# Optimization experiments

Measured on AMD Instinct MI355X. Metric: run time of the kernel, lower is better.

Reference implementation:

```python
import jax, jax.numpy as jnp
import numpy as np

B, L = 16, 54            # dialogues, utterances per dialogue
NDIM = 512; H = 512; NS = 2
T = B * L                # 864 utterances
N = 3 * T                # 2592 nodes (l,a,v per utterance)
NE = B * (L + 3)         # 912 hyperedges (3 modality + L utterance per dialogue)
NNZ = 6 * T              # 5184 incidence entries
E = B * 3 * L * (L - 1)  # 137376 directed intra-modality edges
NUM_L = 3; NUM_K = 4
EPS = 1e-8


def _build_indices():
    rng = np.random.default_rng(0)
    spk = rng.integers(0, NS, size=(B, L))
    # qmask [L, B, NS] one-hot of speakers (matches torch argmax path)
    qmask = np.eye(NS, dtype=np.float32)[spk].transpose(1, 0, 2)
    ar = np.arange(L)
    i1, i2, ht = [], [], []
    for d in range(B):
        base = d * 3 * L
        nl = base + ar; na = nl + L; nv = nl + 2 * L
        # 3 modality hyperedges then L per-utterance (l,a,v) hyperedges
        i1 += [nl, na, nv, np.stack([nl, na, nv], 1).reshape(-1)]
        eb = d * (L + 3)
        i2 += [np.repeat(eb + np.arange(3), L), np.repeat(eb + 3 + ar, 3)]
        ht += [np.ones(L, np.int64), np.zeros(3, np.int64)]
    hyperedge_index = np.stack([np.concatenate(i1), np.concatenate(i2)]).astype(np.int64)
    hyperedge_type = np.concatenate(ht)
    # full permutation edges within each modality of each dialogue
    s0 = np.repeat(ar, L); d0 = np.tile(ar, L)
    m = s0 != d0; s0, d0 = s0[m], d0[m]
    src, dst, et = [], [], []
    for d in range(B):
        same = (spk[d][s0] == spk[d][d0]).astype(np.int64)
        for mm in range(3):
            off = d * 3 * L + mm * L
            src.append(s0 + off); dst.append(d0 + off); et.append(same)
    edge_index = np.stack([np.concatenate(src), np.concatenate(dst)]).astype(np.int64)
    edge_type = np.concatenate(et)
    return qmask, hyperedge_index, hyperedge_type, edge_index, edge_type


def setup_inputs() -> dict:
    key = jax.random.key(0)
    ks = jax.random.split(key, 16)
    qmask, hei, het, ei, et = _build_indices()
    n = lambda k, s: jax.random.normal(k, s, dtype=jnp.float32)
    inp = {
        'a': n(ks[0], (T, NDIM)), 'v': n(ks[1], (T, NDIM)), 'l': n(ks[2], (T, NDIM)),
        'qmask': jnp.asarray(qmask),
        'spk_emb': n(ks[3], (NS, NDIM)) * 0.05,
        'fc1_W': n(ks[4], (NDIM, H)) * 0.05, 'fc1_b': jnp.zeros((H,), jnp.float32),
        'he_weight': jnp.ones((NE,), jnp.float32),
        'ew_weight': jnp.ones((NNZ,), jnp.float32),
        'he_attr1': jax.random.uniform(ks[5], (H,), dtype=jnp.float32),
        'he_attr2': jax.random.uniform(ks[6], (H,), dtype=jnp.float32),
        'hc_W': n(ks[7], (NUM_L, H, H)) * 0.05, 'hc_b': jnp.zeros((NUM_L, H), jnp.float32),
        'm3_W0': n(ks[8], (NUM_K, H, H)) * 0.05,
        'm3_W1': n(ks[9], (NUM_K, H, H)) * 0.05,
        'm3_Wself': n(ks[10], (NUM_K, H, H)) * 0.05,
        'm3_b': jnp.zeros((NUM_K, H), jnp.float32),
        'hyperedge_index': jnp.asarray(hei), 'hyperedge_type': jnp.asarray(het),
        'edge_index': jnp.asarray(ei), 'edge_type': jnp.asarray(et),
    }
    return inp


def reference(a, v, l, qmask, spk_emb, fc1_W, fc1_b, he_weight, ew_weight,
              he_attr1, he_attr2, hc_W, hc_b, m3_W0, m3_W1, m3_Wself, m3_b,
              hyperedge_index, hyperedge_type, edge_index, edge_type):
    seg = jax.ops.segment_sum
    # speaker embedding added to text modality (equal dia_len -> simple transpose)
    qm = qmask.transpose(1, 0, 2).reshape(T, NS)
    l = l + spk_emb[jnp.argmax(qm, axis=-1)]
    # per-dialogue node order: [l_d ; a_d ; v_d]
    feats = jnp.concatenate([l.reshape(B, L, NDIM), a.reshape(B, L, NDIM),
                             v.reshape(B, L, NDIM)], axis=1).reshape(N, NDIM)
    x1 = feats @ fc1_W + fc1_b
    node_i, edge_i = hyperedge_index[0], hyperedge_index[1]
    tfl = hyperedge_type.astype(x1.dtype)[:, None]
    edge_attr = he_attr1[None, :] * tfl + he_attr2[None, :] * (1.0 - tfl)  # [NE,H]
    out = x1
    for ll in range(NUM_L):  # hypergraph conv: gather->edge agg->scatter->linear
        de = seg(ew_weight, edge_i, num_segments=NE)
        e = seg(ew_weight[:, None] * out[node_i], edge_i, num_segments=NE)
        e = e / (de + EPS)[:, None] + edge_attr
        c = he_weight[edge_i]
        dn = seg(c, node_i, num_segments=N)
        agg = seg(c[:, None] * e[edge_i], node_i, num_segments=N) / (dn + EPS)[:, None]
        out = jax.nn.relu(agg @ hc_W[ll] + hc_b[ll])
    src, dst = edge_index[0], edge_index[1]
    same_spk = (edge_type == 1)[:, None]
    deg = seg(jnp.ones_like(dst, dtype=x1.dtype), dst, num_segments=N)
    gnn_out = x1
    denoise = jnp.float32(0.0)
    for kk in range(NUM_K):  # 2-relation RGCN-style denoise layer
        h0 = gnn_out @ m3_W0[kk]
        h1 = gnn_out @ m3_W1[kk]
        msg = jnp.where(same_spk, h1[src], h0[src])
        agg = seg(msg, dst, num_segments=N) / (deg + EPS)[:, None]
        f = jax.nn.relu(agg + gnn_out @ m3_Wself[kk] + m3_b[kk])
        denoise = jnp.mean(f * f)
        gnn_out = gnn_out + f
    return out + gnn_out, denoise
```

## Files before the change

kernel.cpp:

```cpp
#include <hip/hip_runtime.h>

typedef unsigned short ushort_t;
typedef __attribute__((ext_vector_type(4))) float f32x4;
typedef __attribute__((ext_vector_type(8))) short s16x8;
typedef __attribute__((ext_vector_type(8))) unsigned short u16x8;

#define NNODE 2592
#define MATSZ (512*512)
#define INV53 (1.0f/(53.0f + 1e-8f))

__device__ __forceinline__ ushort_t f2b(float f){
  union {unsigned int i; float f;} x; x.f = f;
  unsigned int r = (x.i + 0x7fffu + ((x.i>>16)&1u))>>16;
  return (ushort_t)r;
}

__device__ __forceinline__ void gemm32(const ushort_t* As,
    const ushort_t* W, int col0, f32x4 acc[2][2])
{
  const int tid = threadIdx.x;
  const int wave = tid>>6, lane = tid&63;
  const int ml = lane&15, quad = lane>>4;
  #pragma unroll
  for (int mf=0;mf<2;mf++)
    #pragma unroll
    for (int nf=0;nf<2;nf++) acc[mf][nf] = (f32x4){0.f,0.f,0.f,0.f};

  const ushort_t* bw0 = W + (size_t)(col0 + wave*32 + ml)*512 + quad*8;
  const ushort_t* bw1 = bw0 + (size_t)16*512;
  const int rsw = ml&7;
  #pragma unroll
  for (int ks=0; ks<16; ks++){
    const int chunk = ks*4 + quad;
    const int abase = (chunk>>3)*64 + (((chunk&7) ^ rsw)<<3);
    s16x8 a0 = *(const s16x8*)&As[(size_t)ml*512 + abase];
    s16x8 a1 = *(const s16x8*)&As[(size_t)(16+ml)*512 + abase];
    s16x8 b0 = *(const s16x8*)(bw0 + ks*32);
    s16x8 b1 = *(const s16x8*)(bw1 + ks*32);
    acc[0][0] = __builtin_amdgcn_mfma_f32_16x16x32_bf16(a0,b0,acc[0][0],0,0,0);
    acc[0][1] = __builtin_amdgcn_mfma_f32_16x16x32_bf16(a0,b1,acc[0][1],0,0,0);
    acc[1][0] = __builtin_amdgcn_mfma_f32_16x16x32_bf16(a1,b0,acc[1][0],0,0,0);
    acc[1][1] = __builtin_amdgcn_mfma_f32_16x16x32_bf16(a1,b1,acc[1][1],0,0,0);
  }
}

__device__ __forceinline__ void stageA_flat(ushort_t* As, const float* src, int r0){
  const int tid = threadIdx.x;
  int row = tid>>3, seg = tid&7;
  const float* p = src + (size_t)(r0+row)*512 + seg*64;
  int rsw = row&7;
  ushort_t* dstA = &As[row*512 + seg*64];
  #pragma unroll
  for (int j=0;j<8;j++){
    f32x4 xa = *(const f32x4*)(p+j*8), xb = *(const f32x4*)(p+j*8+4);
    u16x8 v;
    #pragma unroll
    for (int jj=0;jj<4;jj++){ v[jj]=f2b(xa[jj]); v[4+jj]=f2b(xb[jj]); }
    *(u16x8*)&dstA[(j ^ rsw)<<3] = v;
  }
}

__global__ __launch_bounds__(256) void prep_kernel(
    const float* __restrict__ fc1, const float* __restrict__ hc,
    const float* __restrict__ m0, const float* __restrict__ m1,
    const float* __restrict__ ms,
    const float* __restrict__ A_in, const float* __restrict__ V_in,
    const float* __restrict__ L_in, const float* __restrict__ qmask,
    const float* __restrict__ spk,
    ushort_t* __restrict__ WT, float* __restrict__ FS,
    float* __restrict__ cnts, float* __restrict__ acc,
    unsigned int* __restrict__ counter)
{
  __shared__ float tile[64][65];
  __shared__ unsigned char spks[54];
  const int tid = threadIdx.x;
  if (blockIdx.x >= 1024){
    int d = blockIdx.x - 1024;
    if (tid < 54)
      spks[tid] = qmask[(tid*16+d)*2+1] > qmask[(tid*16+d)*2];
    __syncthreads();
    float cnt1 = 0.f;
    #pragma unroll
    for (int i=0;i<54;i++) cnt1 += (float)spks[i];
    float cnt0 = 54.f - cnt1;
    int col = tid*2;
    #pragma unroll
    for (int m=0;m<3;m++){
      float s0x=0.f,s0y=0.f,s1x=0.f,s1y=0.f;
      const float* base = (m==0)?L_in:(m==1)?A_in:V_in;
      for (int i=0;i<54;i++){
        float2 x = *(const float2*)&base[(size_t)(d*54+i)*512 + col];
        if (spks[i]){ s1x+=x.x; s1y+=x.y; } else { s0x+=x.x; s0y+=x.y; }
      }
      if (m==0){
        float2 e0 = *(const float2*)&spk[col];
        float2 e1 = *(const float2*)&spk[512+col];
        s0x += cnt0*e0.x; s0y += cnt0*e0.y;
        s1x += cnt1*e1.x; s1y += cnt1*e1.y;
      }
      float2 o0; o0.x=s0x; o0.y=s0y;
      float2 o1; o1.x=s1x; o1.y=s1y;
      *(float2*)&FS[(size_t)(d*6+m*2  )*512 + col] = o0;
      *(float2*)&FS[(size_t)(d*6+m*2+1)*512 + col] = o1;
    }
    if (tid==0){ cnts[d*2]=cnt0; cnts[d*2+1]=cnt1; }
    return;
  }
  if (blockIdx.x==0 && tid==0){ *acc = 0.f; *counter = 0u; }
  int w = blockIdx.x>>6, t = blockIdx.x&63, bx = t>>3, by = t&7;
  const float* src = (w==0) ? fc1
                   : (w<4)  ? hc + (size_t)(w-1)*MATSZ
                   : (w<8)  ? m0 + (size_t)(w-4)*MATSZ
                   : (w<12) ? m1 + (size_t)(w-8)*MATSZ
                            : ms + (size_t)(w-12)*MATSZ;
  const float* src2 = (w>=12) ? m1 + (size_t)(w-12)*MATSZ : nullptr;
  ushort_t* dst = WT + (size_t)w*MATSZ;
  int r0 = bx*64, c0 = by*64;
  #pragma unroll
  for (int j=0;j<4;j++){
    int idx = j*256 + tid;
    int r = idx>>4, c4 = (idx&15)*4;
    size_t off = (size_t)(r0+r)*512 + c0 + c4;
    f32x4 v = *(const f32x4*)&src[off];
    if (w>=12){
      f32x4 v2 = *(const f32x4*)&src2[off];
      #pragma unroll
      for (int jj=0;jj<4;jj++) v[jj] -= INV53 * v2[jj];
    }
    #pragma unroll
    for (int jj=0;jj<4;jj++) tile[r][c4+jj] = v[jj];
  }
  __syncthreads();
  #pragma unroll
  for (int j=0;j<2;j++){
    int idx = j*256 + tid;
    int c = idx>>3, r8 = (idx&7)*8;
    u16x8 v;
    #pragma unroll
    for (int tt=0;tt<8;tt++) v[tt] = f2b(tile[r8+tt][c]);
    *(u16x8*)&dst[(size_t)(c0+c)*512 + r0 + r8] = v;
  }
}

__global__ __launch_bounds__(256) void fc1_kernel(
    const float* __restrict__ A_in, const float* __restrict__ V_in,
    const float* __restrict__ L_in, const float* __restrict__ qmask,
    const float* __restrict__ spk, const ushort_t* __restrict__ WT,
    const float* __restrict__ fc1_b, float* __restrict__ X1,
    const float* __restrict__ FS, const float* __restrict__ cnts,
    float* __restrict__ Gs)
{
  __shared__ __align__(16) ushort_t As[32*512];
  const int b = blockIdx.x, tid = threadIdx.x;
  const int wave = tid>>6, lane = tid&63;
  const int ml = lane&15, quad = lane>>4;
  if (b < 324){
    const int r0 = (b>>2)*32, col0 = (b&3)*128;
    {
      int row = tid>>3, seg = tid&7, gr = r0+row;
      int d = gr/162, rm = gr-d*162, m = rm/54, i = rm-m*54, t = d*54+i;
      const float* pa = ((m==0)?L_in:(m==1)?A_in:V_in) + (size_t)t*512 + seg*64;
      const float* pb = pa;
      bool hassp = (m==0);
      if (hassp){
        int sp = qmask[(i*16+d)*2+1] > qmask[(i*16+d)*2];
        pb = spk + sp*512 + seg*64;
      }
      int rsw = row&7;
      ushort_t* dstA = &As[row*512 + seg*64];
      #pragma unroll
      for (int j=0;j<8;j++){
        f32x4 xa = *(const f32x4*)(pa+j*8), xb = *(const f32x4*)(pa+j*8+4);
        if (hassp){
          f32x4 ya = *(const f32x4*)(pb+j*8), yb = *(const f32x4*)(pb+j*8+4);
          #pragma unroll
          for (int jj=0;jj<4;jj++){ xa[jj]+=ya[jj]; xb[jj]+=yb[jj]; }
        }
        u16x8 v;
        #pragma unroll
        for (int jj=0;jj<4;jj++){ v[jj]=f2b(xa[jj]); v[4+jj]=f2b(xb[jj]); }
        *(u16x8*)&dstA[(j ^ rsw)<<3] = v;
      }
    }
    __syncthreads();
    f32x4 acc[2][2];
    gemm32(As, WT, col0, acc);
    #pragma unroll
    for (int nf=0;nf<2;nf++){
      int col = col0 + wave*32 + nf*16 + ml;
      float bv = fc1_b[col];
      #pragma unroll
      for (int mf=0;mf<2;mf++)
        #pragma unroll
        for (int r=0;r<4;r++){
          int gr = r0 + mf*16 + quad*4 + r;
          X1[(size_t)gr*512 + col] = acc[mf][nf][r] + bv;
        }
    }
  } else {
    const int bb = b-324;
    const int r0 = (bb>>2)*32, col0 = (bb&3)*128;
    stageA_flat(As, FS, r0);
    __syncthreads();
    f32x4 acc[2][2];
    gemm32(As, WT, col0, acc);
    #pragma unroll
    for (int nf=0;nf<2;nf++){
      int col = col0 + wave*32 + nf*16 + ml;
      float bv = fc1_b[col];
      #pragma unroll
      for (int mf=0;mf<2;mf++)
        #pragma unroll
        for (int r=0;r<4;r++){
          int gr = r0 + mf*16 + quad*4 + r;
          float cw = cnts[(gr/6)*2 + (gr&1)];
          Gs[(size_t)gr*512 + col] = acc[mf][nf][r] + cw*bv;
        }
    }
  }
}

__global__ __launch_bounds__(256) void ka_kernel(int kk,
    const float* __restrict__ gin, const float* __restrict__ Gs,
    const ushort_t* __restrict__ WT, const float* __restrict__ m3_b,
    float* __restrict__ HS, float* __restrict__ Sp,
    const float* __restrict__ edge_src, const float* __restrict__ ew_w,
    const int* __restrict__ het, const float* __restrict__ attr1,
    const float* __restrict__ attr2, float* __restrict__ EB)
{
  __shared__ __align__(16) ushort_t As[32*512];
  const int b = blockIdx.x, tid = threadIdx.x;
  const int wave = tid>>6, lane = tid&63;
  const int ml = lane&15, quad = lane>>4;
  if (b < 324){
    const int r0 = (b>>2)*32, col0 = (b&3)*128;
    stageA_flat(As, gin, r0);
    __syncthreads();
    f32x4 acc[2][2];
    gemm32(As, WT + (size_t)(12+kk)*MATSZ, col0, acc);
    #pragma unroll
    for (int nf=0;nf<2;nf++){
      int col = col0 + wave*32 + nf*16 + ml;
      float bv = m3_b[kk*512 + col];
      #pragma unroll
      for (int mf=0;mf<2;mf++)
        #pragma unroll
        for (int r=0;r<4;r++){
          int gr = r0 + mf*16 + quad*4 + r;
          HS[(size_t)gr*512 + col] = acc[mf][nf][r] + bv;
        }
    }
  } else if (b < 348){
    const int bb = b-324;
    const int rt = bb>>3, c8 = bb&7;
    const int r0 = rt*32, col0 = (c8&3)*128;
    const ushort_t* W = WT + (size_t)((c8<4 ? 4 : 8)+kk)*MATSZ;
    const int cb = (c8<4) ? 0 : 512;
    stageA_flat(As, Gs, r0);
    __syncthreads();
    f32x4 acc[2][2];
    gemm32(As, W, col0, acc);
    #pragma unroll
    for (int nf=0;nf<2;nf++){
      int col = cb + col0 + wave*32 + nf*16 + ml;
      #pragma unroll
      for (int mf=0;mf<2;mf++)
        #pragma unroll
        for (int r=0;r<4;r++){
          int row = r0 + mf*16 + quad*4 + r;
          Sp[(size_t)row*1024 + col] = acc[mf][nf][r];
        }
    }
  } else {
    int e = b - 348;
    int d = e/57, r = e - d*57;
    int col = tid*2;
    float sx=0.f, sy=0.f, de=0.f;
    if (r < 3){
      int nnz0 = d*324 + r*54;
      const float* row = edge_src + ((size_t)(d*162 + r*54))*512 + col;
      for (int i=0;i<54;i++){
        float w = ew_w[nnz0+i];
        float2 x = *(const float2*)row;
        sx += w*x.x; sy += w*x.y; de += w;
        row += 512;
      }
    } else {
      int i = r-3;
      int nnz0 = d*324 + 162 + i*3;
      #pragma unroll
      for (int m=0;m<3;m++){
        float w = ew_w[nnz0+m];
        const float* row = edge_src + ((size_t)(d*162 + m*54 + i))*512 + col;
        float2 x = *(const float2*)row;
        sx += w*x.x; sy += w*x.y; de += w;
      }
    }
    float invde = 1.0f/(de + 1e-8f);
    const float* at = het[e] ? attr1 : attr2;
    float2 o;
    o.x = sx*invde + at[col];
    o.y = sy*invde + at[col+1];
    *(float2*)(EB + (size_t)e*512 + col) = o;
  }
}

template<bool LAST>
__global__ __launch_bounds__(256) void kb_kernel(int lk,
    const float* __restrict__ EB, const ushort_t* __restrict__ WT,
    const float* __restrict__ hc_b, float* __restrict__ dst,
    const float* __restrict__ gin, const float* __restrict__ HS,
    const float* __restrict__ Sp, const float* __restrict__ qmask,
    const float* __restrict__ he_w,
    float* __restrict__ Gout, float* __restrict__ GsOut,
    const float* __restrict__ OUThg, float* __restrict__ dout,
    float* __restrict__ accp, unsigned int* __restrict__ counter)
{
  __shared__ __align__(16) union {
    ushort_t As[32*512];
    struct { unsigned char spks[54]; float red[256]; } sf;
  } sm;
  const int b = blockIdx.x, tid = threadIdx.x;
  if (!LAST && b < 324){
    const int r0 = (b>>2)*32, col0 = (b&3)*128;
    {
      int row = tid>>3, seg = tid&7, gr = r0+row;
      int d = gr/162, rm = gr-d*162, m = rm/54, i = rm-m*54;
      int em = d*57+m, eu = d*57+3+i;
      float w1 = he_w[em], w2 = he_w[eu], inv = 1.0f/(w1+w2+1e-8f);
      float c1 = w1*inv, c2 = w2*inv;
      const float* pa = EB + (size_t)em*512 + seg*64;
      const float* pb = EB + (size_t)eu*512 + seg*64;
      int rsw = row&7;
      ushort_t* dstA = &sm.As[row*512 + seg*64];
      #pragma unroll
      for (int j=0;j<8;j++){
        f32x4 xa = *(const f32x4*)(pa+j*8), xb = *(const f32x4*)(pa+j*8+4);
        f32x4 ya = *(const f32x4*)(pb+j*8), yb = *(const f32x4*)(pb+j*8+4);
        u16x8 v;
        #pragma unroll
        for (int jj=0;jj<4;jj++){
          v[jj]   = f2b(c1*xa[jj] + c2*ya[jj]);
          v[4+jj] = f2b(c1*xb[jj] + c2*yb[jj]);
        }
        *(u16x8*)&dstA[(j ^ rsw)<<3] = v;
      }
    }
    __syncthreads();
    f32x4 acc[2][2];
    gemm32(sm.As, WT + (size_t)(1+lk)*MATSZ, col0, acc);
    const int wave = tid>>6, lane = tid&63;
    const int ml = lane&15, quad = lane>>4;
    #pragma unroll
    for (int nf=0;nf<2;nf++){
      int col = col0 + wave*32 + nf*16 + ml;
      float bv = hc_b[lk*512 + col];
      #pragma unroll
      for (int mf=0;mf<2;mf++)
        #pragma unroll
        for (int r=0;r<4;r++){
          int gr = r0 + mf*16 + quad*4 + r;
          dst[(size_t)gr*512 + col] = fmaxf(acc[mf][nf][r] + bv, 0.f);
        }
    }
  } else {
    const int sfid = LAST ? b : b-324;
    const int g = sfid>>1, d = g/3;
    const int col = (sfid&1)*256 + tid;
    if (tid < 54)
      sm.sf.spks[tid] = qmask[(tid*16+d)*2+1] > qmask[(tid*16+d)*2];
    __syncthreads();
    const float* r0p = Sp + (size_t)(g*2)*1024;
    const float* r1p = Sp + (size_t)(g*2+1)*1024;
    float S1_0 = r0p[512+col];
    float S1_1 = r1p[512+col];
    float S0_0 = r1p[col];
    float S0_1 = r0p[col];
    size_t base = (size_t)g*54*512 + col;
    float gs0=0.f, gs1=0.f, sumsq=0.f;
    for (int i=0;i<54;i++){
      size_t off = base + (size_t)i*512;
      int sp = sm.sf.spks[i];
      float S1 = sp ? S1_1 : S1_0;
      float S0 = sp ? S0_1 : S0_0;
      float hs = HS[off], gi = gin[off];
      float f = fmaxf((S1 + S0)*INV53 + hs, 0.f);
      float gn = gi + f;
      if (LAST){
        sumsq += f*f;
        dout[off] = OUThg[off] + gn;
      } else {
        Gout[off] = gn;
        if (sp) gs1 += gn; else gs0 += gn;
      }
    }
    if (!LAST){
      GsOut[(size_t)(g*2)*512 + col]   = gs0;
      GsOut[(size_t)(g*2+1)*512 + col] = gs1;
    } else {
      sm.sf.red[tid] = sumsq;
      __syncthreads();
      #pragma unroll
      for (int s=128; s>0; s>>=1){
        if (tid < s) sm.sf.red[tid] += sm.sf.red[tid+s];
        __syncthreads();
      }
      if (tid == 0){
        atomicAdd(accp, sm.sf.red[0]);
        __threadfence();
        unsigned int old = atomicAdd(counter, 1u);
        if (old == 95u)
          dout[(size_t)NNODE*512] = atomicAdd(accp, 0.0f) * (1.0f/1327104.0f);
      }
    }
  }
}

extern "C" void kernel_launch(void* const* d_in, const int* in_sizes, int n_in,
                              void* d_out, int out_size, void* d_ws, size_t ws_size,
                              hipStream_t stream)
{
  const float* A_in   = (const float*)d_in[0];
  const float* V_in   = (const float*)d_in[1];
  const float* L_in   = (const float*)d_in[2];
  const float* qmask  = (const float*)d_in[3];
  const float* spk    = (const float*)d_in[4];
  const float* fc1_W  = (const float*)d_in[5];
  const float* fc1_b  = (const float*)d_in[6];
  const float* he_w   = (const float*)d_in[7];
  const float* ew_w   = (const float*)d_in[8];
  const float* attr1  = (const float*)d_in[9];
  const float* attr2  = (const float*)d_in[10];
  const float* hc_W   = (const float*)d_in[11];
  const float* hc_b   = (const float*)d_in[12];
  const float* m3_W0  = (const float*)d_in[13];
  const float* m3_W1  = (const float*)d_in[14];
  const float* m3_Ws  = (const float*)d_in[15];
  const float* m3_b   = (const float*)d_in[16];
  const int*   het    = (const int*)d_in[18];
  float* dout = (float*)d_out;

  char* ws = (char*)d_ws;
  ushort_t* WT = (ushort_t*)ws;
  float* X1 = (float*)(ws + (size_t)16*MATSZ*2);
  float* OA = X1 + (size_t)NNODE*512;
  float* OB = OA + (size_t)NNODE*512;
  float* OC = OB + (size_t)NNODE*512;
  float* GA = OC + (size_t)NNODE*512;
  float* GB = GA + (size_t)NNODE*512;
  float* HS = GB + (size_t)NNODE*512;
  float* EB = HS + (size_t)NNODE*512;
  float* Sp = EB + (size_t)912*512;
  float* Gs = Sp + 96*1024;
  float* FS = Gs + 96*512;
  float* cnts = FS + 96*512;
  float* acc = cnts + 32;
  unsigned int* counter = (unsigned int*)(acc + 1);

  prep_kernel<<<1040,256,0,stream>>>(fc1_W, hc_W, m3_W0, m3_W1, m3_Ws,
                                     A_in, V_in, L_in, qmask, spk,
                                     WT, FS, cnts, acc, counter);
  fc1_kernel<<<336,256,0,stream>>>(A_in, V_in, L_in, qmask, spk, WT, fc1_b,
                                   X1, FS, cnts, Gs);

  ka_kernel<<<1260,256,0,stream>>>(0, X1, Gs, WT, m3_b, HS, Sp,
                                   X1, ew_w, het, attr1, attr2, EB);
  kb_kernel<false><<<420,256,0,stream>>>(0, EB, WT, hc_b, OA, X1, HS, Sp,
      qmask, he_w, GA, Gs, nullptr, nullptr, acc, counter);
  ka_kernel<<<1260,256,0,stream>>>(1, GA, Gs, WT, m3_b, HS, Sp,
                                   OA, ew_w, het, attr1, attr2, EB);
  kb_kernel<false><<<420,256,0,stream>>>(1, EB, WT, hc_b, OB, GA, HS, Sp,
      qmask, he_w, GB, Gs, nullptr, nullptr, acc, counter);
  ka_kernel<<<1260,256,0,stream>>>(2, GB, Gs, WT, m3_b, HS, Sp,
                                   OB, ew_w, het, attr1, attr2, EB);
  kb_kernel<false><<<420,256,0,stream>>>(2, EB, WT, hc_b, OC, GB, HS, Sp,
      qmask, he_w, GA, Gs, nullptr, nullptr, acc, counter);
  ka_kernel<<<348,256,0,stream>>>(3, GA, Gs, WT, m3_b, HS, Sp,
                                  X1, ew_w, het, attr1, attr2, EB);
  kb_kernel<true><<<96,256,0,stream>>>(3, EB, WT, hc_b, nullptr, GA, HS, Sp,
      qmask, he_w, nullptr, nullptr, OC, dout, acc, counter);

  (void)in_sizes; (void)n_in; (void)out_size; (void)ws_size;
}
```

Before: 260.7 us.

## Overlap weight transposes with fc1 GEMM by moving them into fc1 kernel

The prep kernel now converts and transposes only the fc1 weight and computes the speaker feature sums. Conversion of the other 15 weight matrices moves into extra blocks of the fc1 kernel, which share its LDS through a union. This lets those transposes run alongside the fc1 GEMM instead of in a serial kernel before it, shortening the critical path. The cost is a larger fc1 grid with mixed block roles, which adds some contention.

```diff
diff --git a/kernel.cpp b/kernel.cpp
--- a/kernel.cpp
+++ b/kernel.cpp
@@ -60,61 +60,10 @@
   }
 }
 
-__global__ __launch_bounds__(256) void prep_kernel(
-    const float* __restrict__ fc1, const float* __restrict__ hc,
-    const float* __restrict__ m0, const float* __restrict__ m1,
-    const float* __restrict__ ms,
-    const float* __restrict__ A_in, const float* __restrict__ V_in,
-    const float* __restrict__ L_in, const float* __restrict__ qmask,
-    const float* __restrict__ spk,
-    ushort_t* __restrict__ WT, float* __restrict__ FS,
-    float* __restrict__ cnts, float* __restrict__ acc,
-    unsigned int* __restrict__ counter)
-{
-  __shared__ float tile[64][65];
-  __shared__ unsigned char spks[54];
+__device__ __forceinline__ void transpose_tile(float (*tile)[65],
+    const float* src, const float* src2, ushort_t* dst, int bx, int by)
+{
   const int tid = threadIdx.x;
-  if (blockIdx.x >= 1024){
-    int d = blockIdx.x - 1024;
-    if (tid < 54)
-      spks[tid] = qmask[(tid*16+d)*2+1] > qmask[(tid*16+d)*2];
-    __syncthreads();
-    float cnt1 = 0.f;
-    #pragma unroll
-    for (int i=0;i<54;i++) cnt1 += (float)spks[i];
-    float cnt0 = 54.f - cnt1;
-    int col = tid*2;
-    #pragma unroll
-    for (int m=0;m<3;m++){
-      float s0x=0.f,s0y=0.f,s1x=0.f,s1y=0.f;
-      const float* base = (m==0)?L_in:(m==1)?A_in:V_in;
-      for (int i=0;i<54;i++){
-        float2 x = *(const float2*)&base[(size_t)(d*54+i)*512 + col];
-        if (spks[i]){ s1x+=x.x; s1y+=x.y; } else { s0x+=x.x; s0y+=x.y; }
-      }
-      if (m==0){
-        float2 e0 = *(const float2*)&spk[col];
-        float2 e1 = *(const float2*)&spk[512+col];
-        s0x += cnt0*e0.x; s0y += cnt0*e0.y;
-        s1x += cnt1*e1.x; s1y += cnt1*e1.y;
-      }
-      float2 o0; o0.x=s0x; o0.y=s0y;
-      float2 o1; o1.x=s1x; o1.y=s1y;
-      *(float2*)&FS[(size_t)(d*6+m*2  )*512 + col] = o0;
-      *(float2*)&FS[(size_t)(d*6+m*2+1)*512 + col] = o1;
-    }
-    if (tid==0){ cnts[d*2]=cnt0; cnts[d*2+1]=cnt1; }
-    return;
-  }
-  if (blockIdx.x==0 && tid==0){ *acc = 0.f; *counter = 0u; }
-  int w = blockIdx.x>>6, t = blockIdx.x&63, bx = t>>3, by = t&7;
-  const float* src = (w==0) ? fc1
-                   : (w<4)  ? hc + (size_t)(w-1)*MATSZ
-                   : (w<8)  ? m0 + (size_t)(w-4)*MATSZ
-                   : (w<12) ? m1 + (size_t)(w-8)*MATSZ
-                            : ms + (size_t)(w-12)*MATSZ;
-  const float* src2 = (w>=12) ? m1 + (size_t)(w-12)*MATSZ : nullptr;
-  ushort_t* dst = WT + (size_t)w*MATSZ;
   int r0 = bx*64, c0 = by*64;
   #pragma unroll
   for (int j=0;j<4;j++){
@@ -122,7 +71,7 @@
     int r = idx>>4, c4 = (idx&15)*4;
     size_t off = (size_t)(r0+r)*512 + c0 + c4;
     f32x4 v = *(const f32x4*)&src[off];
-    if (w>=12){
+    if (src2){
       f32x4 v2 = *(const f32x4*)&src2[off];
       #pragma unroll
       for (int jj=0;jj<4;jj++) v[jj] -= INV53 * v2[jj];
@@ -142,18 +91,84 @@
   }
 }
 
+__global__ __launch_bounds__(256) void prep0_kernel(
+    const float* __restrict__ fc1,
+    const float* __restrict__ A_in, const float* __restrict__ V_in,
+    const float* __restrict__ L_in, const float* __restrict__ qmask,
+    const float* __restrict__ spk,
+    ushort_t* __restrict__ WT, float* __restrict__ FS,
+    float* __restrict__ cnts, float* __restrict__ acc,
+    unsigned int* __restrict__ counter)
+{
+  __shared__ float tile[64][65];
+  __shared__ unsigned char spks[54];
+  const int tid = threadIdx.x;
+  if (blockIdx.x >= 64){
+    int d = blockIdx.x - 64;
+    if (tid < 54)
+      spks[tid] = qmask[(tid*16+d)*2+1] > qmask[(tid*16+d)*2];
+    __syncthreads();
+    float cnt1 = 0.f;
+    #pragma unroll
+    for (int i=0;i<54;i++) cnt1 += (float)spks[i];
+    float cnt0 = 54.f - cnt1;
+    int col = tid*2;
+    #pragma unroll
+    for (int m=0;m<3;m++){
+      float s0x=0.f,s0y=0.f,s1x=0.f,s1y=0.f;
+      const float* base = (m==0)?L_in:(m==1)?A_in:V_in;
+      for (int i=0;i<54;i++){
+        float2 x = *(const float2*)&base[(size_t)(d*54+i)*512 + col];
+        if (spks[i]){ s1x+=x.x; s1y+=x.y; } else { s0x+=x.x; s0y+=x.y; }
+      }
+      if (m==0){
+        float2 e0 = *(const float2*)&spk[col];
+        float2 e1 = *(const float2*)&spk[512+col];
+        s0x += cnt0*e0.x; s0y += cnt0*e0.y;
+        s1x += cnt1*e1.x; s1y += cnt1*e1.y;
+      }
+      float2 o0; o0.x=s0x; o0.y=s0y;
+      float2 o1; o1.x=s1x; o1.y=s1y;
+      *(float2*)&FS[(size_t)(d*6+m*2  )*512 + col] = o0;
+      *(float2*)&FS[(size_t)(d*6+m*2+1)*512 + col] = o1;
+    }
+    if (tid==0){ cnts[d*2]=cnt0; cnts[d*2+1]=cnt1; }
+    return;
+  }
+  if (blockIdx.x==0 && tid==0){ *acc = 0.f; *counter = 0u; }
+  int t = blockIdx.x;
+  transpose_tile(tile, fc1, nullptr, WT, t>>3, t&7);
+}
+
 __global__ __launch_bounds__(256) void fc1_kernel(
     const float* __restrict__ A_in, const float* __restrict__ V_in,
     const float* __restrict__ L_in, const float* __restrict__ qmask,
-    const float* __restrict__ spk, const ushort_t* __restrict__ WT,
+    const float* __restrict__ spk, const ushort_t* __restrict__ WTc,
+    ushort_t* __restrict__ WT,
+    const float* __restrict__ hc, const float* __restrict__ m0,
+    const float* __restrict__ m1, const float* __restrict__ ms,
     const float* __restrict__ fc1_b, float* __restrict__ X1,
     const float* __restrict__ FS, const float* __restrict__ cnts,
     float* __restrict__ Gs)
 {
-  __shared__ __align__(16) ushort_t As[32*512];
+  __shared__ __align__(16) union {
+    ushort_t As[32*512];
+    float tile[64][65];
+  } sm;
   const int b = blockIdx.x, tid = threadIdx.x;
   const int wave = tid>>6, lane = tid&63;
   const int ml = lane&15, quad = lane>>4;
+  if (b >= 336){
+    const int bb = b - 336;
+    const int w = 1 + (bb>>6), t = bb&63;
+    const float* src = (w<4)  ? hc + (size_t)(w-1)*MATSZ
+                     : (w<8)  ? m0 + (size_t)(w-4)*MATSZ
+                     : (w<12) ? m1 + (size_t)(w-8)*MATSZ
+                              : ms + (size_t)(w-12)*MATSZ;
+    const float* src2 = (w>=12) ? m1 + (size_t)(w-12)*MATSZ : nullptr;
+    transpose_tile(sm.tile, src, src2, WT + (size_t)w*MATSZ, t>>3, t&7);
+    return;
+  }
   if (b < 324){
     const int r0 = (b>>2)*32, col0 = (b&3)*128;
     {
@@ -167,7 +182,7 @@
         pb = spk + sp*512 + seg*64;
       }
       int rsw = row&7;
-      ushort_t* dstA = &As[row*512 + seg*64];
+      ushort_t* dstA = &sm.As[row*512 + seg*64];
       #pragma unroll
       for (int j=0;j<8;j++){
         f32x4 xa = *(const f32x4*)(pa+j*8), xb = *(const f32x4*)(pa+j*8+4);
@@ -184,7 +199,7 @@
     }
     __syncthreads();
     f32x4 acc[2][2];
-    gemm32(As, WT, col0, acc);
+    gemm32(sm.As, WTc, col0, acc);
     #pragma unroll
     for (int nf=0;nf<2;nf++){
       int col = col0 + wave*32 + nf*16 + ml;
@@ -200,10 +215,10 @@
   } else {
     const int bb = b-324;
     const int r0 = (bb>>2)*32, col0 = (bb&3)*128;
-    stageA_flat(As, FS, r0);
+    stageA_flat(sm.As, FS, r0);
     __syncthreads();
     f32x4 acc[2][2];
-    gemm32(As, WT, col0, acc);
+    gemm32(sm.As, WTc, col0, acc);
     #pragma unroll
     for (int nf=0;nf<2;nf++){
       int col = col0 + wave*32 + nf*16 + ml;
@@ -457,11 +472,11 @@
   float* acc = cnts + 32;
   unsigned int* counter = (unsigned int*)(acc + 1);
 
-  prep_kernel<<<1040,256,0,stream>>>(fc1_W, hc_W, m3_W0, m3_W1, m3_Ws,
-                                     A_in, V_in, L_in, qmask, spk,
-                                     WT, FS, cnts, acc, counter);
-  fc1_kernel<<<336,256,0,stream>>>(A_in, V_in, L_in, qmask, spk, WT, fc1_b,
-                                   X1, FS, cnts, Gs);
+  prep0_kernel<<<80,256,0,stream>>>(fc1_W, A_in, V_in, L_in, qmask, spk,
+                                    WT, FS, cnts, acc, counter);
+  fc1_kernel<<<1296,256,0,stream>>>(A_in, V_in, L_in, qmask, spk, WT, WT,
+                                    hc_W, m3_W0, m3_W1, m3_Ws, fc1_b,
+                                    X1, FS, cnts, Gs);
 
   ka_kernel<<<1260,256,0,stream>>>(0, X1, Gs, WT, m3_b, HS, Sp,
                                    X1, ew_w, het, attr1, attr2, EB);
```

Result: slower. 296.3 us (+13.6%).
